# Performance work log

Measured on AMD Instinct MI355X. Metric: run time of the kernel, lower is better.

Reference implementation:

```python
import jax, jax.numpy as jnp
import numpy as np

N_NODES = 65536
N_EDGES = 524288
N_GRAPHS = 1024
NODES_PER_GRAPH = N_NODES // N_GRAPHS
FD = 78  # num_features_xd


def _lin(key, fan_in, fan_out):
    kw, kb = jax.random.split(key)
    s = 1.0 / np.sqrt(fan_in)
    return (jax.random.uniform(kw, (fan_in, fan_out), jnp.float32, -s, s),
            jax.random.uniform(kb, (fan_out,), jnp.float32, -s, s))


def setup_inputs() -> dict:
    key = jax.random.key(0)
    ks = jax.random.split(key, 32)
    inp = {}
    inp["x1"] = jax.random.normal(ks[0], (N_NODES, FD), jnp.float32)
    inp["edge_index1"] = jax.random.randint(ks[1], (2, N_EDGES), 0, N_NODES)
    inp["batch1"] = jnp.arange(N_NODES) // NODES_PER_GRAPH
    inp["x2"] = jax.random.normal(ks[2], (N_NODES, FD), jnp.float32)
    inp["edge_index2"] = jax.random.randint(ks[3], (2, N_EDGES), 0, N_NODES)
    inp["batch2"] = jnp.arange(N_NODES) // NODES_PER_GRAPH
    inp["target"] = jax.random.normal(ks[4], (N_GRAPHS, 1000), jnp.float32)
    # GCN + MLP params for both drug streams
    for i, pre in enumerate(["d1", "d2"]):
        base = 5 + i * 5
        inp[f"{pre}_w1"], inp[f"{pre}_b1"] = _lin(ks[base + 0], FD, FD)
        inp[f"{pre}_w2"], inp[f"{pre}_b2"] = _lin(ks[base + 1], FD, FD * 2)
        inp[f"{pre}_w3"], inp[f"{pre}_b3"] = _lin(ks[base + 2], FD * 2, FD * 4)
        inp[f"{pre}_fc1_w"], inp[f"{pre}_fc1_b"] = _lin(ks[base + 3], FD * 4, 1024)
        inp[f"{pre}_fc2_w"], inp[f"{pre}_fc2_b"] = _lin(ks[base + 4], 1024, 64)
    inp["xt_w"], inp["xt_b"] = _lin(ks[15], 1000, 128)
    inp["fc1_w"], inp["fc1_b"] = _lin(ks[16], 256, 128)
    inp["fc2_w"], inp["fc2_b"] = _lin(ks[17], 128, 32)
    inp["out_w"], inp["out_b"] = _lin(ks[18], 32, 1)
    return inp


def _deg_inv_sqrt(dst, n_nodes):
    # degree with self-loops (PyG add_self_loops then symmetric norm)
    deg = jax.ops.segment_sum(jnp.ones(dst.shape[0], jnp.float32), dst,
                              num_segments=n_nodes) + 1.0
    return jax.lax.rsqrt(deg)


def _gcn_conv(x, w, b, src, dst, dinv):
    # h = X W; out_i = sum_j norm_ij h_j (+ self-loop) + b
    h = x @ w
    coef = dinv[src] * dinv[dst]                      # [E]
    msg = h[src] * coef[:, None]                      # [E, F] gather
    agg = jax.ops.segment_sum(msg, dst, num_segments=x.shape[0])
    agg = agg + h * (dinv * dinv)[:, None]            # self-loop term
    return agg + b


def _drug_branch(x, edge_index, batch, w1, b1, w2, b2, w3, b3,
                 fc1_w, fc1_b, fc2_w, fc2_b):
    src, dst = edge_index[0], edge_index[1]
    dinv = _deg_inv_sqrt(dst, x.shape[0])
    x = jax.nn.relu(_gcn_conv(x, w1, b1, src, dst, dinv))
    x = jax.nn.relu(_gcn_conv(x, w2, b2, src, dst, dinv))
    x = jax.nn.relu(_gcn_conv(x, w3, b3, src, dst, dinv))
    x = jax.ops.segment_max(x, batch, num_segments=N_GRAPHS)  # global max pool
    x = jax.nn.relu(x @ fc1_w + fc1_b)
    # dropout = identity (eval mode)
    return x @ fc2_w + fc2_b


def reference(x1, edge_index1, batch1, x2, edge_index2, batch2, target,
              d1_w1, d1_b1, d1_w2, d1_b2, d1_w3, d1_b3,
              d1_fc1_w, d1_fc1_b, d1_fc2_w, d1_fc2_b,
              d2_w1, d2_b1, d2_w2, d2_b2, d2_w3, d2_b3,
              d2_fc1_w, d2_fc1_b, d2_fc2_w, d2_fc2_b,
              xt_w, xt_b, fc1_w, fc1_b, fc2_w, fc2_b, out_w, out_b):
    g1 = _drug_branch(x1, edge_index1, batch1, d1_w1, d1_b1, d1_w2, d1_b2,
                      d1_w3, d1_b3, d1_fc1_w, d1_fc1_b, d1_fc2_w, d1_fc2_b)
    g2 = _drug_branch(x2, edge_index2, batch2, d2_w1, d2_b1, d2_w2, d2_b2,
                      d2_w3, d2_b3, d2_fc1_w, d2_fc1_b, d2_fc2_w, d2_fc2_b)
    xd = jnp.concatenate([g1, g2], axis=1)            # [G, 128]
    xt = target.reshape(-1, 1000) @ xt_w + xt_b       # [G, 128]
    xc = jnp.concatenate([xd, xt], axis=1)            # [G, 256]
    xc = jax.nn.relu(xc @ fc1_w + fc1_b)
    xc = jax.nn.relu(xc @ fc2_w + fc2_b)
    return xc @ out_w + out_b                         # [G, 1]
```

## Files before the change

kernel.cpp:

```cpp
#include <hip/hip_runtime.h>
#include <hip/hip_bf16.h>
#include <math.h>

#define N_NODES 65536
#define N_EDGES 524288
#define N_GRAPHS 1024
#define NPG 64
#define FD 78
#define RPS 65600
#define BCAP 3072
#define EPB 4096

typedef __attribute__((ext_vector_type(8))) short bf16x8;
typedef __attribute__((ext_vector_type(4))) float f32x4;

__device__ __forceinline__ unsigned short f2bf(float v) {
    unsigned int u = __float_as_uint(v);
    unsigned int r = (u + 0x7FFFu + ((u >> 16) & 1u)) >> 16;
    return (unsigned short)r;
}
__device__ __forceinline__ float bf2f(unsigned short h) {
    return __uint_as_float(((unsigned int)h) << 16);
}

__global__ __launch_bounds__(256, 3) void gemm_mfma(
    const unsigned short* __restrict__ Ah, const unsigned short* __restrict__ Al,
    const unsigned short* __restrict__ Wh0, const unsigned short* __restrict__ Wl0,
    const unsigned short* __restrict__ Wh1, const unsigned short* __restrict__ Wl1,
    const float* __restrict__ bias0, const float* __restrict__ bias1,
    float* __restrict__ Cf, unsigned short* __restrict__ Ch, unsigned short* __restrict__ Cl,
    int N, int Kp, int ldc, int relu, int zpad, int omode, int brshift)
{
    __shared__ __align__(16) unsigned short sAh[128][40];
    __shared__ __align__(16) unsigned short sAl[128][40];
    __shared__ __align__(16) unsigned short sBh[128][40];
    __shared__ __align__(16) unsigned short sBl[128][40];

    int tid = threadIdx.x;
    int bm = blockIdx.y << 7;
    int bn = blockIdx.x << 7;
    int b = blockIdx.y >> brshift;
    const unsigned short* Wh = b ? Wh1 : Wh0;
    const unsigned short* Wl = b ? Wl1 : Wl0;
    const float* bias = b ? bias1 : bias0;

    int lane = tid & 63;
    int wid = tid >> 6;
    int wr = wid >> 1, wc = wid & 1;
    int cr = lane & 15;
    int kg = lane >> 4;

    int r0 = tid >> 2;
    int sg = (tid & 3) * 8;
    const unsigned short* pAh = Ah + (size_t)(bm + r0) * Kp + sg;
    const unsigned short* pAl = Al + (size_t)(bm + r0) * Kp + sg;
    const unsigned short* pBh = Wh + (size_t)(bn + r0) * Kp + sg;
    const unsigned short* pBl = Wl + (size_t)(bn + r0) * Kp + sg;
    size_t rstep = (size_t)64 * Kp;

    uint4 vAh0, vAh1, vAl0, vAl1, vBh0, vBh1, vBl0, vBl1;
    auto LOADT = [&](int k0) {
        vAh0 = *(const uint4*)(pAh + k0);
        vAh1 = *(const uint4*)(pAh + k0 + rstep);
        vAl0 = *(const uint4*)(pAl + k0);
        vAl1 = *(const uint4*)(pAl + k0 + rstep);
        vBh0 = *(const uint4*)(pBh + k0);
        vBh1 = *(const uint4*)(pBh + k0 + rstep);
        vBl0 = *(const uint4*)(pBl + k0);
        vBl1 = *(const uint4*)(pBl + k0 + rstep);
    };
    auto WRITET = [&]() {
        *(uint4*)&sAh[r0][sg] = vAh0;
        *(uint4*)&sAh[r0 + 64][sg] = vAh1;
        *(uint4*)&sAl[r0][sg] = vAl0;
        *(uint4*)&sAl[r0 + 64][sg] = vAl1;
        *(uint4*)&sBh[r0][sg] = vBh0;
        *(uint4*)&sBh[r0 + 64][sg] = vBh1;
        *(uint4*)&sBl[r0][sg] = vBl0;
        *(uint4*)&sBl[r0 + 64][sg] = vBl1;
    };

    f32x4 acc[4][4] = {};

    LOADT(0);
    WRITET();
    __syncthreads();

    for (int k0 = 0; k0 < Kp; k0 += 32) {
        int more = (k0 + 32) < Kp;
        if (more) LOADT(k0 + 32);

        bf16x8 bH[4], bL[4];
        #pragma unroll
        for (int nf = 0; nf < 4; ++nf) {
            bH[nf] = *(const bf16x8*)&sBh[wc * 64 + nf * 16 + cr][kg * 8];
            bL[nf] = *(const bf16x8*)&sBl[wc * 64 + nf * 16 + cr][kg * 8];
        }
        #pragma unroll
        for (int mf = 0; mf < 4; ++mf) {
            bf16x8 aH = *(const bf16x8*)&sAh[wr * 64 + mf * 16 + cr][kg * 8];
            bf16x8 aL = *(const bf16x8*)&sAl[wr * 64 + mf * 16 + cr][kg * 8];
            #pragma unroll
            for (int nf = 0; nf < 4; ++nf) {
                acc[mf][nf] = __builtin_amdgcn_mfma_f32_16x16x32_bf16(aH, bH[nf], acc[mf][nf], 0, 0, 0);
                acc[mf][nf] = __builtin_amdgcn_mfma_f32_16x16x32_bf16(aH, bL[nf], acc[mf][nf], 0, 0, 0);
                acc[mf][nf] = __builtin_amdgcn_mfma_f32_16x16x32_bf16(aL, bH[nf], acc[mf][nf], 0, 0, 0);
            }
        }
        __syncthreads();
        if (more) {
            WRITET();
            __syncthreads();
        }
    }

    if (omode == 2) {
        int g = (blockIdx.y << 1) + wr;
        #pragma unroll
        for (int nf = 0; nf < 4; ++nf) {
            int col = bn + wc * 64 + nf * 16 + cr;
            if (col < N) {
                float m = -INFINITY;
                #pragma unroll
                for (int mf = 0; mf < 4; ++mf) {
                    f32x4 v = acc[mf][nf];
                    #pragma unroll
                    for (int j = 0; j < 4; ++j) m = fmaxf(m, v[j]);
                }
                m = fmaxf(m + bias[col], 0.f);
                m = fmaxf(m, __shfl_xor(m, 16, 64));
                m = fmaxf(m, __shfl_xor(m, 32, 64));
                if (kg == 0)
                    atomicMax((unsigned int*)&Cf[(size_t)g * ldc + col], __float_as_uint(m));
            }
        }
        return;
    }

    #pragma unroll
    for (int mf = 0; mf < 4; ++mf) {
        int rowbase = bm + wr * 64 + mf * 16 + kg * 4;
        #pragma unroll
        for (int nf = 0; nf < 4; ++nf) {
            int col = bn + wc * 64 + nf * 16 + cr;
            if (col >= ldc) continue;
            int live = col < N;
            if (!live && !zpad) continue;
            float bv = live ? bias[col] : 0.f;
            f32x4 v = acc[mf][nf];
            #pragma unroll
            for (int j = 0; j < 4; ++j) {
                size_t idx = (size_t)(rowbase + j) * ldc + col;
                float o = v[j] + bv;
                if (relu) o = fmaxf(o, 0.f);
                if (!live) o = 0.f;
                if (omode == 0) {
                    Cf[idx] = o;
                } else {
                    unsigned short h = f2bf(o);
                    Ch[idx] = h;
                    Cl[idx] = f2bf(o - bf2f(h));
                }
            }
        }
    }
}

__global__ __launch_bounds__(256) void gemm_mfma_sk(
    const unsigned short* __restrict__ Ah, const unsigned short* __restrict__ Al,
    const unsigned short* __restrict__ Wh0, const unsigned short* __restrict__ Wl0,
    const unsigned short* __restrict__ Wh1, const unsigned short* __restrict__ Wl1,
    const float* __restrict__ bias0, const float* __restrict__ bias1,
    float* __restrict__ C, int Kp, int ldc, int kchunk, int brshift, int colstep)
{
    __shared__ __align__(16) unsigned short sAh[128][40];
    __shared__ __align__(16) unsigned short sAl[128][40];
    __shared__ __align__(16) unsigned short sBh[64][40];
    __shared__ __align__(16) unsigned short sBl[64][40];

    int tid = threadIdx.x;
    int bm = blockIdx.y << 7;
    int bn = blockIdx.x << 6;
    int b = blockIdx.y >> brshift;
    const unsigned short* Wh = b ? Wh1 : Wh0;
    const unsigned short* Wl = b ? Wl1 : Wl0;
    const float* bias = b ? bias1 : bias0;
    int rowoff = bm - (b << 10);
    int kbase = blockIdx.z * kchunk;
    int lane = tid & 63;
    int wid = tid >> 6;
    int wr = wid >> 1, wc = wid & 1;
    int cr = lane & 15;
    int kg = lane >> 4;

    f32x4 acc[4][2] = {};

    for (int k0 = kbase; k0 < kbase + kchunk; k0 += 32) {
        #pragma unroll
        for (int s = tid; s < 512; s += 256) {
            int r = s >> 2, seg = s & 3;
            *(uint4*)&sAh[r][seg * 8] =
                *(const uint4*)(Ah + (size_t)(bm + r) * Kp + k0 + seg * 8);
        }
        #pragma unroll
        for (int s = tid; s < 512; s += 256) {
            int r = s >> 2, seg = s & 3;
            *(uint4*)&sAl[r][seg * 8] =
                *(const uint4*)(Al + (size_t)(bm + r) * Kp + k0 + seg * 8);
        }
        {
            int r = tid >> 2, seg = tid & 3;
            *(uint4*)&sBh[r][seg * 8] =
                *(const uint4*)(Wh + (size_t)(bn + r) * Kp + k0 + seg * 8);
            *(uint4*)&sBl[r][seg * 8] =
                *(const uint4*)(Wl + (size_t)(bn + r) * Kp + k0 + seg * 8);
        }
        __syncthreads();

        bf16x8 bH[2], bL[2];
        #pragma unroll
        for (int nf = 0; nf < 2; ++nf) {
            bH[nf] = *(const bf16x8*)&sBh[wc * 32 + nf * 16 + cr][kg * 8];
            bL[nf] = *(const bf16x8*)&sBl[wc * 32 + nf * 16 + cr][kg * 8];
        }
        #pragma unroll
        for (int mf = 0; mf < 4; ++mf) {
            bf16x8 aH = *(const bf16x8*)&sAh[wr * 64 + mf * 16 + cr][kg * 8];
            bf16x8 aL = *(const bf16x8*)&sAl[wr * 64 + mf * 16 + cr][kg * 8];
            #pragma unroll
            for (int nf = 0; nf < 2; ++nf) {
                acc[mf][nf] = __builtin_amdgcn_mfma_f32_16x16x32_bf16(aH, bH[nf], acc[mf][nf], 0, 0, 0);
                acc[mf][nf] = __builtin_amdgcn_mfma_f32_16x16x32_bf16(aH, bL[nf], acc[mf][nf], 0, 0, 0);
                acc[mf][nf] = __builtin_amdgcn_mfma_f32_16x16x32_bf16(aL, bH[nf], acc[mf][nf], 0, 0, 0);
            }
        }
        __syncthreads();
    }

    int z0 = blockIdx.z == 0;
    #pragma unroll
    for (int mf = 0; mf < 4; ++mf) {
        int rowbase = rowoff + wr * 64 + mf * 16 + kg * 4;
        #pragma unroll
        for (int nf = 0; nf < 2; ++nf) {
            int cl = bn + wc * 32 + nf * 16 + cr;
            float bv = z0 ? bias[cl] : 0.f;
            int col = b * colstep + cl;
            f32x4 v = acc[mf][nf];
            #pragma unroll
            for (int j = 0; j < 4; ++j)
                atomicAdd(&C[(size_t)(rowbase + j) * ldc + col], v[j] + bv);
        }
    }
}

struct PrepDesc { const float* W; unsigned short* Wh; unsigned short* Wl; int K, N, Kp, Np; };
struct PrepArgs { PrepDesc d[11]; };

__global__ void prep_all(PrepArgs pa) {
    PrepDesc de = pa.d[blockIdx.y];
    int tot = de.Np * de.Kp;
    for (int t = blockIdx.x * blockDim.x + threadIdx.x; t < tot; t += gridDim.x * blockDim.x) {
        int n = t / de.Kp, k = t - n * de.Kp;
        float v = (n < de.N && k < de.K) ? de.W[(size_t)k * de.N + n] : 0.f;
        unsigned short h = f2bf(v);
        de.Wh[t] = h;
        de.Wl[t] = f2bf(v - bf2f(h));
    }
}

__global__ void split_pad(const float* __restrict__ x, unsigned short* __restrict__ Xh,
                          unsigned short* __restrict__ Xl, int M, int F, int Kp) {
    int t = blockIdx.x * blockDim.x + threadIdx.x;
    if (t >= M * Kp) return;
    int i = t / Kp, c = t - i * Kp;
    float v = (c < F) ? x[(size_t)i * F + c] : 0.f;
    unsigned short h = f2bf(v);
    Xh[t] = h;
    Xl[t] = f2bf(v - bf2f(h));
}

__global__ __launch_bounds__(256) void fc_row(
    const float* __restrict__ A, const float* __restrict__ B,
    const float* __restrict__ bias, float* __restrict__ C,
    int M, int N, int K, int lda, int ldc, int relu)
{
    int nchunks = (N + 63) >> 6;
    int bid = blockIdx.x;
    int nc = bid % nchunks;
    int m = ((bid / nchunks) << 2) + (threadIdx.x >> 6);
    int lane = threadIdx.x & 63;
    if (m >= M) return;
    int n = (nc << 6) + lane;
    int nclamp = n < N ? n : N - 1;
    const float* __restrict__ a = A + (size_t)m * lda;
    const float* __restrict__ bp = B + nclamp;
    float acc = 0.f;
    int kk = 0;
    #pragma unroll 4
    for (; kk + 4 <= K; kk += 4) {
        float a0 = a[kk + 0], a1 = a[kk + 1], a2 = a[kk + 2], a3 = a[kk + 3];
        float b0 = bp[(size_t)(kk + 0) * N];
        float b1 = bp[(size_t)(kk + 1) * N];
        float b2 = bp[(size_t)(kk + 2) * N];
        float b3 = bp[(size_t)(kk + 3) * N];
        acc = fmaf(a0, b0, acc);
        acc = fmaf(a1, b1, acc);
        acc = fmaf(a2, b2, acc);
        acc = fmaf(a3, b3, acc);
    }
    for (; kk < K; ++kk)
        acc = fmaf(a[kk], bp[(size_t)kk * N], acc);
    if (n < N) {
        float v = acc + bias[n];
        if (relu) v = fmaxf(v, 0.f);
        C[(size_t)m * ldc + n] = v;
    }
}

__global__ __launch_bounds__(1024) void bucket_scatter(
    const int* __restrict__ s1, const int* __restrict__ d1,
    const int* __restrict__ s2, const int* __restrict__ d2,
    int* __restrict__ bcnt, unsigned int* __restrict__ bbuf, int E)
{
    __shared__ int lhist[256];
    __shared__ int lbase[256];
    int nblk = E / EPB;
    int b = blockIdx.x >= nblk;
    int blk = blockIdx.x - b * nblk;
    const int* sp = b ? s2 : s1;
    const int* dp = b ? d2 : d1;
    int e0 = blk * EPB;
    if (threadIdx.x < 256) lhist[threadIdx.x] = 0;
    __syncthreads();

    unsigned int pack[EPB / 1024];
    int bkt[EPB / 1024], rank[EPB / 1024];
    #pragma unroll
    for (int i = 0; i < EPB / 1024; ++i) {
        int e = e0 + threadIdx.x + i * 1024;
        int s = sp[e], d = dp[e];
        bkt[i] = d >> 8;
        pack[i] = ((unsigned int)s << 8) | (unsigned int)(d & 255);
        rank[i] = atomicAdd(&lhist[bkt[i]], 1);
    }
    __syncthreads();
    if (threadIdx.x < 256) {
        int c = lhist[threadIdx.x];
        lbase[threadIdx.x] = c ? atomicAdd(&bcnt[(b << 8) | threadIdx.x], c) : 0;
    }
    __syncthreads();
    #pragma unroll
    for (int i = 0; i < EPB / 1024; ++i) {
        int pos = lbase[bkt[i]] + rank[i];
        if (pos < BCAP)
            bbuf[(size_t)((b << 8) | bkt[i]) * BCAP + pos] = pack[i];
    }
}

__global__ __launch_bounds__(256) void bucket_count(const int* __restrict__ bcnt,
                                                    const unsigned int* __restrict__ bbuf,
                                                    int* __restrict__ cntB) {
    __shared__ int lc[256];
    int bk = blockIdx.x;
    lc[threadIdx.x] = 0;
    __syncthreads();
    int n = bcnt[bk]; if (n > BCAP) n = BCAP;
    const unsigned int* p = bbuf + (size_t)bk * BCAP;
    for (int i = threadIdx.x; i < n; i += 256)
        atomicAdd(&lc[p[i] & 255u], 1);
    __syncthreads();
    int br = bk >> 8, nb = (bk & 255) << 8;
    cntB[br * N_NODES + nb + threadIdx.x] = lc[threadIdx.x];
}

__global__ __launch_bounds__(256) void bucket_sort(const int* __restrict__ bcnt,
                                                   const unsigned int* __restrict__ bbuf,
                                                   const int* __restrict__ rowpB,
                                                   int* __restrict__ csrsB) {
    __shared__ int lrow[256];
    __shared__ int lcur[256];
    int bk = blockIdx.x;
    int br = bk >> 8, nb = (bk & 255) << 8;
    lrow[threadIdx.x] = rowpB[br * RPS + nb + threadIdx.x];
    lcur[threadIdx.x] = 0;
    __syncthreads();
    int n = bcnt[bk]; if (n > BCAP) n = BCAP;
    const unsigned int* p = bbuf + (size_t)bk * BCAP;
    int* outp = csrsB + (size_t)br * N_EDGES;
    for (int i = threadIdx.x; i < n; i += 256) {
        unsigned int e = p[i];
        int dl = e & 255u;
        int pos = lrow[dl] + atomicAdd(&lcur[dl], 1);
        outp[pos] = (int)(e >> 8);
    }
}

__global__ void make_dinv2(const int* __restrict__ cnt, float* __restrict__ dinv) {
    int t = blockIdx.x * blockDim.x + threadIdx.x;
    if (t < 2 * N_NODES) dinv[t] = rsqrtf((float)cnt[t] + 1.0f);
}

__global__ __launch_bounds__(1024) void scan_rowptr(const int* __restrict__ cntB,
                                                    int* __restrict__ rowpB) {
    __shared__ int sums[1024];
    const int* cnt = cntB + blockIdx.x * N_NODES;
    int* row_ptr = rowpB + blockIdx.x * RPS;
    int t = threadIdx.x;
    int base = t * 64;
    int s = 0;
    #pragma unroll 4
    for (int i = 0; i < 64; ++i) s += cnt[base + i];
    sums[t] = s;
    __syncthreads();
    for (int off = 1; off < 1024; off <<= 1) {
        int v = sums[t];
        int add = (t >= off) ? sums[t - off] : 0;
        __syncthreads();
        sums[t] = v + add;
        __syncthreads();
    }
    int run = (t == 0) ? 0 : sums[t - 1];
    for (int i = 0; i < 64; ++i) {
        row_ptr[base + i] = run;
        run += cnt[base + i];
    }
    if (t == 1023) row_ptr[N_NODES] = run;
}

__global__ void repack_pad2(const float* __restrict__ x1, const float* __restrict__ x2,
                            float* __restrict__ xp) {
    int t = blockIdx.x * blockDim.x + threadIdx.x;
    int total = 2 * N_NODES * 80;
    if (t >= total) return;
    int i = t / 80, c = t - i * 80;
    int b = i >> 16, il = i & 65535;
    const float* x = b ? x2 : x1;
    xp[t] = (c < FD) ? x[(size_t)il * FD + c] : 0.f;
}

__global__ __launch_bounds__(256) void gather8(
    const float* __restrict__ x, const int* __restrict__ rowpB,
    const int* __restrict__ csrsB, const float* __restrict__ dinvB,
    unsigned short* __restrict__ Ah, unsigned short* __restrict__ Al,
    int S, int Kp)
{
    int Kp8 = Kp >> 3;
    int t = blockIdx.x * blockDim.x + threadIdx.x;
    int total = 2 * N_NODES * Kp8;
    if (t >= total) return;
    int i = t / Kp8;
    int g = t - i * Kp8;
    int f = g << 3;
    size_t ob = (size_t)i * Kp + f;
    if (f >= S) {
        bf16x8 z = {};
        *(bf16x8*)&Ah[ob] = z;
        *(bf16x8*)&Al[ob] = z;
        return;
    }
    int b = i >> 16, il = i & 65535;
    const int* rowp = rowpB + b * RPS;
    const int* csrs = csrsB + (size_t)b * N_EDGES;
    const float* dinv = dinvB + ((size_t)b << 16);
    const float* xb = x + (((size_t)b << 16) * S);
    float di = dinv[il];
    const float* xr = x + (size_t)i * S + f;
    f32x4 s0 = *(const f32x4*)xr;
    f32x4 s1 = *(const f32x4*)(xr + 4);
    float w = di * di;
    s0 *= w;
    s1 *= w;
    int p0 = rowp[il], p1 = rowp[il + 1];
    int p = p0;
    for (; p + 4 <= p1; p += 4) {
        int sa = csrs[p], sb = csrs[p + 1], sc = csrs[p + 2], sd = csrs[p + 3];
        float ca = dinv[sa] * di, cb = dinv[sb] * di;
        float cc = dinv[sc] * di, cd = dinv[sd] * di;
        const float* ra = xb + (size_t)sa * S + f;
        const float* rb = xb + (size_t)sb * S + f;
        const float* rc = xb + (size_t)sc * S + f;
        const float* rd = xb + (size_t)sd * S + f;
        f32x4 a0 = *(const f32x4*)ra, a1 = *(const f32x4*)(ra + 4);
        f32x4 b0 = *(const f32x4*)rb, b1 = *(const f32x4*)(rb + 4);
        f32x4 c0 = *(const f32x4*)rc, c1 = *(const f32x4*)(rc + 4);
        f32x4 d0 = *(const f32x4*)rd, d1 = *(const f32x4*)(rd + 4);
        s0 += ca * a0 + cb * b0 + cc * c0 + cd * d0;
        s1 += ca * a1 + cb * b1 + cc * c1 + cd * d1;
    }
    for (; p < p1; ++p) {
        int sa = csrs[p];
        float ca = dinv[sa] * di;
        const float* ra = xb + (size_t)sa * S + f;
        s0 += ca * *(const f32x4*)ra;
        s1 += ca * *(const f32x4*)(ra + 4);
    }
    bf16x8 hh, ll;
    #pragma unroll
    for (int j = 0; j < 4; ++j) {
        unsigned short h0 = f2bf(s0[j]);
        hh[j] = (short)h0;
        ll[j] = (short)f2bf(s0[j] - bf2f(h0));
        unsigned short h1 = f2bf(s1[j]);
        hh[4 + j] = (short)h1;
        ll[4 + j] = (short)f2bf(s1[j] - bf2f(h1));
    }
    *(bf16x8*)&Ah[ob] = hh;
    *(bf16x8*)&Al[ob] = ll;
}

static inline void fc_launch(const float* A, const float* B, const float* bias, float* C,
                             int M, int N, int K, int lda, int ldc, int relu, hipStream_t s) {
    int nchunks = (N + 63) / 64;
    int mblocks = (M + 3) / 4;
    fc_row<<<nchunks * mblocks, 256, 0, s>>>(A, B, bias, C, M, N, K, lda, ldc, relu);
}

extern "C" void kernel_launch(void* const* d_in, const int* in_sizes, int n_in,
                              void* d_out, int out_size, void* d_ws, size_t ws_size,
                              hipStream_t stream) {
    (void)in_sizes; (void)n_in; (void)out_size; (void)ws_size;

    const float* x1     = (const float*)d_in[0];
    const int*   ei1    = (const int*)d_in[1];
    const float* x2     = (const float*)d_in[3];
    const int*   ei2    = (const int*)d_in[4];
    const float* target = (const float*)d_in[6];

    const float* xt_w  = (const float*)d_in[27];
    const float* xt_b  = (const float*)d_in[28];
    const float* fc1_w = (const float*)d_in[29];
    const float* fc1_b = (const float*)d_in[30];
    const float* fc2_w = (const float*)d_in[31];
    const float* fc2_b = (const float*)d_in[32];
    const float* out_w = (const float*)d_in[33];
    const float* out_b = (const float*)d_in[34];

    char* ws = (char*)d_ws;
    unsigned short* AhB = (unsigned short*)(ws + 0);
    unsigned short* AlB = (unsigned short*)(ws + 41943040);
    float* R1   = (float*)(ws + 83886080);
    float* Y2   = (float*)(ws + 83886080);
    char*  FCS  = ws + 83886080;
    int*   csrsB = (int*) (ws + 167772160);
    int*   rowpB = (int*) (ws + 171966464);
    int*   cntB  = (int*) (ws + 172491264);
    float* dinvB = (float*)(ws + 173015552);
    float* xc   = (float*)(ws + 173539840);
    float* xc1  = (float*)(ws + 174588416);
    float* xc2  = (float*)(ws + 175112704);
    unsigned short* wt    = (unsigned short*)(ws + 175243776);
    unsigned short* wtfc1 = (unsigned short*)(ws + 176030208);
    unsigned short* wtfc2 = (unsigned short*)(ws + 178651648);
    unsigned short* wtxt  = (unsigned short*)(ws + 179700224);

    unsigned int* bbuf = (unsigned int*)AhB;
    int*          bcnt = (int*)AlB;

    float* xpad = R1;
    float* y1   = R1;
    float* y2   = Y2;
    float*          pooled = (float*)(FCS + 0);
    unsigned short* Ph = (unsigned short*)(FCS + 2621440);
    unsigned short* Pl = (unsigned short*)(FCS + 3932160);
    unsigned short* Fh = (unsigned short*)(FCS + 5242880);
    unsigned short* Fl = (unsigned short*)(FCS + 9437184);
    unsigned short* Th = (unsigned short*)(FCS + 13631488);
    unsigned short* Tl = (unsigned short*)(FCS + 15728640);

    const int E = N_EDGES;

    const int Ks[3]  = { FD, FD, FD * 2 };
    const int Ns[3]  = { FD, FD * 2, FD * 4 };
    const int Kps[3] = { 96, 96, 160 };
    const int Nps[3] = { 128, 256, 384 };
    const int Ss[3]  = { 80, 80, 160 };
    const int Ldc[3] = { 80, 160, 320 };
    const int wtoff[3] = { 0, 24576, 73728 };
    const int WT_BRANCH = 196608;

    PrepArgs pa;
    for (int br = 0; br < 2; ++br) {
        int base = 7 + br * 10;
        for (int c = 0; c < 3; ++c) {
            unsigned short* wh = wt + br * WT_BRANCH + wtoff[c];
            pa.d[br * 3 + c] = { (const float*)d_in[base + 2 * c], wh,
                                 wh + Nps[c] * Kps[c], Ks[c], Ns[c], Kps[c], Nps[c] };
        }
        pa.d[6 + br] = { (const float*)d_in[base + 6], wtfc1 + br * 655360,
                         wtfc1 + br * 655360 + 327680, FD * 4, 1024, 320, 1024 };
        pa.d[8 + br] = { (const float*)d_in[base + 8], wtfc2 + br * 262144,
                         wtfc2 + br * 262144 + 131072, 1024, 64, 1024, 128 };
    }
    pa.d[10] = { xt_w, wtxt, wtxt + 131072, 1000, 128, 1024, 128 };
    prep_all<<<dim3(256, 11), 256, 0, stream>>>(pa);

    const int* src1 = ei1, *dst1 = ei1 + E;
    const int* src2 = ei2, *dst2 = ei2 + E;
    hipMemsetAsync(bcnt, 0, 512 * sizeof(int), stream);
    bucket_scatter<<<2 * (E / EPB), 1024, 0, stream>>>(src1, dst1, src2, dst2, bcnt, bbuf, E);
    bucket_count<<<512, 256, 0, stream>>>(bcnt, bbuf, cntB);
    make_dinv2<<<(2 * N_NODES + 255) / 256, 256, 0, stream>>>(cntB, dinvB);
    scan_rowptr<<<2, 1024, 0, stream>>>(cntB, rowpB);
    bucket_sort<<<512, 256, 0, stream>>>(bcnt, bbuf, rowpB, csrsB);

    hipMemsetAsync(xc, 0, N_GRAPHS * 256 * sizeof(float), stream);

    repack_pad2<<<(2 * N_NODES * 80 + 255) / 256, 256, 0, stream>>>(x1, x2, xpad);

    const float* cin[3]  = { xpad, y1, y2 };
    float*       cout[3] = { y1, y2, pooled };
    const float* biasc[2][3];
    for (int br = 0; br < 2; ++br) {
        int base = 7 + br * 10;
        biasc[br][0] = (const float*)d_in[base + 1];
        biasc[br][1] = (const float*)d_in[base + 3];
        biasc[br][2] = (const float*)d_in[base + 5];
    }

    for (int c = 0; c < 3; ++c) {
        int Kp = Kps[c], Np = Nps[c], S = Ss[c];
        int total = 2 * N_NODES * (Kp >> 3);
        gather8<<<(total + 255) / 256, 256, 0, stream>>>(
            cin[c], rowpB, csrsB, dinvB, AhB, AlB, S, Kp);
        unsigned short* wh0 = wt + wtoff[c];
        unsigned short* wh1 = wt + WT_BRANCH + wtoff[c];
        if (c == 2) {
            hipMemsetAsync(pooled, 0, 2048 * 320 * sizeof(float), stream);
            gemm_mfma<<<dim3(Np / 128, 1024), 256, 0, stream>>>(
                AhB, AlB, wh0, wh0 + Np * Kp, wh1, wh1 + Np * Kp,
                biasc[0][2], biasc[1][2],
                pooled, nullptr, nullptr, Ns[c], Kp, 320, 1, 0, 2, 9);
        } else {
            gemm_mfma<<<dim3(Np / 128, 1024), 256, 0, stream>>>(
                AhB, AlB, wh0, wh0 + Np * Kp, wh1, wh1 + Np * Kp,
                biasc[0][c], biasc[1][c],
                cout[c], nullptr, nullptr, Ns[c], Kp, Ldc[c], 1, 1, 0, 9);
        }
    }

    split_pad<<<(2048 * 320 + 255) / 256, 256, 0, stream>>>(pooled, Ph, Pl, 2048, 320, 320);
    gemm_mfma<<<dim3(8, 16), 256, 0, stream>>>(
        Ph, Pl, wtfc1, wtfc1 + 327680, wtfc1 + 655360, wtfc1 + 655360 + 327680,
        (const float*)d_in[7 + 7], (const float*)d_in[17 + 7],
        nullptr, Fh, Fl, 1024, 320, 1024, 1, 1, 1, 3);
    gemm_mfma_sk<<<dim3(1, 16, 8), 256, 0, stream>>>(
        Fh, Fl, wtfc2, wtfc2 + 131072, wtfc2 + 262144, wtfc2 + 262144 + 131072,
        (const float*)d_in[7 + 9], (const float*)d_in[17 + 9],
        xc, 1024, 256, 128, 3, 64);

    split_pad<<<(1024 * 1024 + 255) / 256, 256, 0, stream>>>(target, Th, Tl, 1024, 1000, 1024);
    gemm_mfma_sk<<<dim3(2, 8, 8), 256, 0, stream>>>(
        Th, Tl, wtxt, wtxt + 131072, wtxt, wtxt + 131072, xt_b, xt_b,
        xc + 128, 1024, 256, 128, 30, 0);

    fc_launch(xc,  fc1_w, fc1_b, xc1, N_GRAPHS, 128, 256, 256, 128, 1, stream);
    fc_launch(xc1, fc2_w, fc2_b, xc2, N_GRAPHS, 32, 128, 128, 32, 1, stream);
    fc_launch(xc2, out_w, out_b, (float*)d_out, N_GRAPHS, 1, 32, 32, 1, 0, stream);
}
```

Measured before the change: 519.2 us.

## Pack source degree into CSR entries and remap GEMM blocks across XCDs

The CSR sort now stores each edge's source index and source in-degree packed into one 32-bit word. The gather kernel can then compute the normalization with rsqrt inline instead of doing a dependent random load from dinv per edge. Separately, the MFMA GEMM remaps block IDs so that consecutive row tiles land on the same XCD, improving L2 locality for A and W tiles. The packing assumes node indices and degrees fit in 16 bits, which holds for 65536 nodes only if degree stays below 65536. The sort also gains a random read of cnt[s].

```diff
diff --git a/kernel.cpp b/kernel.cpp
--- a/kernel.cpp
+++ b/kernel.cpp
@@ -37,9 +37,16 @@
     __shared__ __align__(16) unsigned short sBl[128][40];
 
     int tid = threadIdx.x;
-    int bm = blockIdx.y << 7;
-    int bn = blockIdx.x << 7;
-    int b = blockIdx.y >> brshift;
+    int nbx = gridDim.x, nby = gridDim.y;
+    int bid = blockIdx.y * nbx + blockIdx.x;
+    int xcd = bid & 7;
+    int j = bid >> 3;
+    int by = xcd * (nby >> 3) + j / nbx;
+    int bx = j % nbx;
+
+    int bm = by << 7;
+    int bn = bx << 7;
+    int b = by >> brshift;
     const unsigned short* Wh = b ? Wh1 : Wh0;
     const unsigned short* Wl = b ? Wl1 : Wl0;
     const float* bias = b ? bias1 : bias0;
@@ -115,7 +122,7 @@
     }
 
     if (omode == 2) {
-        int g = (blockIdx.y << 1) + wr;
+        int g = (by << 1) + wr;
         #pragma unroll
         for (int nf = 0; nf < 4; ++nf) {
             int col = bn + wc * 64 + nf * 16 + cr;
@@ -125,7 +132,7 @@
                 for (int mf = 0; mf < 4; ++mf) {
                     f32x4 v = acc[mf][nf];
                     #pragma unroll
-                    for (int j = 0; j < 4; ++j) m = fmaxf(m, v[j]);
+                    for (int j2 = 0; j2 < 4; ++j2) m = fmaxf(m, v[j2]);
                 }
                 m = fmaxf(m + bias[col], 0.f);
                 m = fmaxf(m, __shfl_xor(m, 16, 64));
@@ -149,9 +156,9 @@
             float bv = live ? bias[col] : 0.f;
             f32x4 v = acc[mf][nf];
             #pragma unroll
-            for (int j = 0; j < 4; ++j) {
-                size_t idx = (size_t)(rowbase + j) * ldc + col;
-                float o = v[j] + bv;
+            for (int j2 = 0; j2 < 4; ++j2) {
+                size_t idx = (size_t)(rowbase + j2) * ldc + col;
+                float o = v[j2] + bv;
                 if (relu) o = fmaxf(o, 0.f);
                 if (!live) o = 0.f;
                 if (omode == 0) {
@@ -377,7 +384,8 @@
 __global__ __launch_bounds__(256) void bucket_sort(const int* __restrict__ bcnt,
                                                    const unsigned int* __restrict__ bbuf,
                                                    const int* __restrict__ rowpB,
-                                                   int* __restrict__ csrsB) {
+                                                   const int* __restrict__ cntB,
+                                                   unsigned int* __restrict__ csrsB) {
     __shared__ int lrow[256];
     __shared__ int lcur[256];
     int bk = blockIdx.x;
@@ -387,12 +395,14 @@
     __syncthreads();
     int n = bcnt[bk]; if (n > BCAP) n = BCAP;
     const unsigned int* p = bbuf + (size_t)bk * BCAP;
-    int* outp = csrsB + (size_t)br * N_EDGES;
+    unsigned int* outp = csrsB + (size_t)br * N_EDGES;
+    const int* cnt = cntB + br * N_NODES;
     for (int i = threadIdx.x; i < n; i += 256) {
         unsigned int e = p[i];
         int dl = e & 255u;
+        int s = (int)(e >> 8);
         int pos = lrow[dl] + atomicAdd(&lcur[dl], 1);
-        outp[pos] = (int)(e >> 8);
+        outp[pos] = ((unsigned int)s << 16) | (unsigned int)(cnt[s] & 0xFFFF);
     }
 }
 
@@ -441,7 +451,7 @@
 
 __global__ __launch_bounds__(256) void gather8(
     const float* __restrict__ x, const int* __restrict__ rowpB,
-    const int* __restrict__ csrsB, const float* __restrict__ dinvB,
+    const unsigned int* __restrict__ csrsB, const float* __restrict__ dinvB,
     unsigned short* __restrict__ Ah, unsigned short* __restrict__ Al,
     int S, int Kp)
 {
@@ -461,7 +471,7 @@
     }
     int b = i >> 16, il = i & 65535;
     const int* rowp = rowpB + b * RPS;
-    const int* csrs = csrsB + (size_t)b * N_EDGES;
+    const unsigned int* csrs = csrsB + (size_t)b * N_EDGES;
     const float* dinv = dinvB + ((size_t)b << 16);
     const float* xb = x + (((size_t)b << 16) * S);
     float di = dinv[il];
@@ -474,9 +484,12 @@
     int p0 = rowp[il], p1 = rowp[il + 1];
     int p = p0;
     for (; p + 4 <= p1; p += 4) {
-        int sa = csrs[p], sb = csrs[p + 1], sc = csrs[p + 2], sd = csrs[p + 3];
-        float ca = dinv[sa] * di, cb = dinv[sb] * di;
-        float cc = dinv[sc] * di, cd = dinv[sd] * di;
+        unsigned int ea = csrs[p], eb = csrs[p + 1], ec = csrs[p + 2], ed = csrs[p + 3];
+        int sa = ea >> 16, sb = eb >> 16, sc = ec >> 16, sd = ed >> 16;
+        float ca = rsqrtf((float)(ea & 0xFFFFu) + 1.0f) * di;
+        float cb = rsqrtf((float)(eb & 0xFFFFu) + 1.0f) * di;
+        float cc = rsqrtf((float)(ec & 0xFFFFu) + 1.0f) * di;
+        float cd = rsqrtf((float)(ed & 0xFFFFu) + 1.0f) * di;
         const float* ra = xb + (size_t)sa * S + f;
         const float* rb = xb + (size_t)sb * S + f;
         const float* rc = xb + (size_t)sc * S + f;
@@ -489,8 +502,9 @@
         s1 += ca * a1 + cb * b1 + cc * c1 + cd * d1;
     }
     for (; p < p1; ++p) {
-        int sa = csrs[p];
-        float ca = dinv[sa] * di;
+        unsigned int ea = csrs[p];
+        int sa = ea >> 16;
+        float ca = rsqrtf((float)(ea & 0xFFFFu) + 1.0f) * di;
         const float* ra = xb + (size_t)sa * S + f;
         s0 += ca * *(const f32x4*)ra;
         s1 += ca * *(const f32x4*)(ra + 4);
@@ -542,7 +556,7 @@
     float* R1   = (float*)(ws + 83886080);
     float* Y2   = (float*)(ws + 83886080);
     char*  FCS  = ws + 83886080;
-    int*   csrsB = (int*) (ws + 167772160);
+    unsigned int* csrsB = (unsigned int*)(ws + 167772160);
     int*   rowpB = (int*) (ws + 171966464);
     int*   cntB  = (int*) (ws + 172491264);
     float* dinvB = (float*)(ws + 173015552);
@@ -602,7 +616,7 @@
     bucket_count<<<512, 256, 0, stream>>>(bcnt, bbuf, cntB);
     make_dinv2<<<(2 * N_NODES + 255) / 256, 256, 0, stream>>>(cntB, dinvB);
     scan_rowptr<<<2, 1024, 0, stream>>>(cntB, rowpB);
-    bucket_sort<<<512, 256, 0, stream>>>(bcnt, bbuf, rowpB, csrsB);
+    bucket_sort<<<512, 256, 0, stream>>>(bcnt, bbuf, rowpB, cntB, csrsB);
 
     hipMemsetAsync(xc, 0, N_GRAPHS * 256 * sizeof(float), stream);
 
```

After: 505.3 us. 2.7% less time.
